# Optimization experiments

Hardware: AMD Instinct MI355X
Metric: run time of the kernel (lower is better)

The kernel has to match this reference:

```python
import jax, jax.numpy as jnp
import numpy as np

N, D, H = 2048, 1024, 16
HD = D // H  # 64
SCALE = float(np.sqrt(HD))  # sqrt(features // heads) = 8.0


def setup_inputs() -> dict:
    key = jax.random.key(0)
    ks = jax.random.split(key, 9)
    s = 0.02
    return {
        "x": jax.random.normal(ks[0], (N, D), dtype=jnp.float32),
        "Wq": jax.random.normal(ks[1], (D, D), dtype=jnp.float32) * s,
        "bq": jnp.zeros((D,), dtype=jnp.float32),
        "Wk": jax.random.normal(ks[2], (D, D), dtype=jnp.float32) * s,
        "bk": jnp.zeros((D,), dtype=jnp.float32),
        "Wv": jax.random.normal(ks[3], (D, D), dtype=jnp.float32) * s,
        "bv": jnp.zeros((D,), dtype=jnp.float32),
        "Wo": jax.random.normal(ks[4], (D, D), dtype=jnp.float32) * s,
        "bo": jnpp if False else jnp.zeros((D,), dtype=jnp.float32),
    }


def reference(x, Wq, bq, Wk, bk, Wv, bv, Wo, bo):
    # projections: [n, d]
    q = x @ Wq + bq
    k = x @ Wk + bk
    v = x @ Wv + bv
    # split heads: n (h d) -> h n d
    def split(t):
        return t.reshape(N, H, HD).transpose(1, 0, 2)
    q, k, v = split(q), split(k), split(v)
    # attention scores [h, n, n]
    scores = jnp.einsum('hnd,hmd->hnm', q, k) / SCALE
    # causal mask (tril), fill with dtype min as in original
    dmin = jnp.finfo(scores.dtype).min
    mask = jnp.tril(jnp.ones((N, N), dtype=bool))
    scores = jnp.where(mask, scores, dmin)
    attn = jax.nn.softmax(scores, axis=-1)
    # weighted sum, merge heads: h n d -> n (h d)
    out = jnp.einsum('hnm,hmd->hnd', attn, v)
    out = out.transpose(1, 0, 2).reshape(N, D)
    return out @ Wo + bo
```

## Files before the change

kernel.cpp:

```cpp
#include <hip/hip_runtime.h>
#include <hip/hip_bf16.h>
#include <math.h>

#define SA_N 2048
#define SA_D 1024
#define SA_H 16
#define SA_HD 64

typedef __attribute__((ext_vector_type(8))) short bf16x8;
typedef __attribute__((ext_vector_type(4))) float f32x4;
typedef __attribute__((address_space(3))) void lds_t;
typedef __attribute__((address_space(1))) void gmem_t;

#define SC2 0.18033688011112042f

__global__ __launch_bounds__(256) void prep_kernel(
    const float* __restrict__ x,
    const float* __restrict__ Wq, const float* __restrict__ Wk,
    const float* __restrict__ Wv, const float* __restrict__ Wo,
    __hip_bfloat16* __restrict__ xbf, __hip_bfloat16* __restrict__ WtAll)
{
    const int tid = threadIdx.x;
    const int z = blockIdx.z;
    if (z < 2) {
        const int r = z * 1024 + blockIdx.y * 32 + (tid >> 3);
        const int c = blockIdx.x * 32 + (tid & 7) * 4;
        const size_t idx = (size_t)r * SA_D + c;
        float4 v = *reinterpret_cast<const float4*>(&x[idx]);
        union { __hip_bfloat16 hh[4]; short4 s4; } u;
        u.hh[0] = __float2bfloat16(v.x);
        u.hh[1] = __float2bfloat16(v.y);
        u.hh[2] = __float2bfloat16(v.z);
        u.hh[3] = __float2bfloat16(v.w);
        *reinterpret_cast<short4*>(&xbf[idx]) = u.s4;
    } else {
        const int w = z - 2;
        const float* W = (w == 0) ? Wq : (w == 1) ? Wk : (w == 2) ? Wv : Wo;
        const float scale = (w == 0) ? SC2 : 1.0f;
        __hip_bfloat16* Wt = WtAll + (size_t)w * SA_D * SA_D;
        __shared__ float t[32][33];
        const int c0 = blockIdx.x * 32, r0 = blockIdx.y * 32;
        const int tx = tid & 31, ty = tid >> 5;
#pragma unroll
        for (int p = 0; p < 4; ++p)
            t[ty + p * 8][tx] = W[(size_t)(r0 + ty + p * 8) * SA_D + c0 + tx] * scale;
        __syncthreads();
#pragma unroll
        for (int p = 0; p < 4; ++p)
            Wt[(size_t)(c0 + ty + p * 8) * SA_D + r0 + tx] =
                __float2bfloat16(t[tx][ty + p * 8]);
    }
}

__global__ __launch_bounds__(256) void gemm_qkv_kernel(
    const __hip_bfloat16* __restrict__ xbf, const __hip_bfloat16* __restrict__ WtAll,
    const float* __restrict__ bq, const float* __restrict__ bk, const float* __restrict__ bv,
    __hip_bfloat16* __restrict__ Qb, __hip_bfloat16* __restrict__ Kb,
    __hip_bfloat16* __restrict__ VtT)
{
    __shared__ __align__(16) char As[64 * 128];
    __shared__ __align__(16) char Bs[3][32 * 128];

    const int tid = threadIdx.x;
    const int wave = tid >> 6, lane = tid & 63;
    const int m = lane & 15, quad = lane >> 4;
    const int wm = wave >> 1, wn = wave & 1;
    const int row0 = blockIdx.y * 64, col0 = blockIdx.x * 32;

    f32x4 acc[3][2];
#pragma unroll
    for (int w = 0; w < 3; ++w)
#pragma unroll
        for (int mi = 0; mi < 2; ++mi) acc[w][mi] = (f32x4){0.f, 0.f, 0.f, 0.f};

    const int sr = tid >> 3;
    const int sc = tid & 7;

    for (int k0 = 0; k0 < SA_D; k0 += 64) {
#pragma unroll
        for (int p = 0; p < 2; ++p) {
            const int r = p * 32 + sr;
            const int pc = (sc ^ (r & 7)) * 16;
            const char* ga = (const char*)(xbf + (size_t)(row0 + r) * SA_D + k0) + pc;
            __builtin_amdgcn_global_load_lds((gmem_t*)ga,
                (lds_t*)(As + p * 4096 + wave * 1024), 16, 0, 0);
        }
#pragma unroll
        for (int w = 0; w < 3; ++w) {
            const int pc = (sc ^ (sr & 7)) * 16;
            const char* gb = (const char*)(WtAll + (size_t)w * SA_D * SA_D
                                           + (size_t)(col0 + sr) * SA_D + k0) + pc;
            __builtin_amdgcn_global_load_lds((gmem_t*)gb,
                (lds_t*)(Bs[w] + wave * 1024), 16, 0, 0);
        }
        __syncthreads();

#pragma unroll
        for (int s = 0; s < 2; ++s) {
            bf16x8 af[2];
#pragma unroll
            for (int mi = 0; mi < 2; ++mi) {
                const int row = wm * 32 + mi * 16 + m;
                const int pc = (s * 4 + quad) ^ (row & 7);
                af[mi] = *reinterpret_cast<const bf16x8*>(As + row * 128 + pc * 16);
            }
            const int rb = wn * 16 + m;
            const int pcb = (s * 4 + quad) ^ (rb & 7);
#pragma unroll
            for (int w = 0; w < 3; ++w) {
                bf16x8 bf = *reinterpret_cast<const bf16x8*>(Bs[w] + rb * 128 + pcb * 16);
#pragma unroll
                for (int mi = 0; mi < 2; ++mi)
                    acc[w][mi] = __builtin_amdgcn_mfma_f32_16x16x32_bf16(
                        af[mi], bf, acc[w][mi], 0, 0, 0);
            }
        }
        __syncthreads();
    }

    const int col = col0 + wn * 16 + m;
    const float bvq = bq[col] * SC2, bvk = bk[col], bvv = bv[col];
#pragma unroll
    for (int mi = 0; mi < 2; ++mi) {
        const int rbase = row0 + wm * 32 + mi * 16 + quad * 4;
#pragma unroll
        for (int reg = 0; reg < 4; ++reg) {
            Qb[(size_t)(rbase + reg) * SA_D + col] = __float2bfloat16(acc[0][mi][reg] + bvq);
            Kb[(size_t)(rbase + reg) * SA_D + col] = __float2bfloat16(acc[1][mi][reg] + bvk);
        }
#pragma unroll
        for (int reg = 0; reg < 4; ++reg) {
            const int jp = (quad * 4 + reg) * 4 + (wm * 2 + mi);
            VtT[(size_t)col * SA_N + row0 + jp] = __float2bfloat16(acc[2][mi][reg] + bvv);
        }
    }
}

__global__ __launch_bounds__(256) void gemm_out_kernel(
    const __hip_bfloat16* __restrict__ A, const __hip_bfloat16* __restrict__ Bt,
    const float* __restrict__ bias, float* __restrict__ Cout)
{
    __shared__ __align__(16) char As[64 * 128];
    __shared__ __align__(16) char Bs[64 * 128];
    const int tid = threadIdx.x;
    const int wave = tid >> 6, lane = tid & 63;
    const int m = lane & 15, quad = lane >> 4;
    const int wm = wave >> 1, wn = wave & 1;
    const int row0 = blockIdx.y * 64, col0 = blockIdx.x * 64;

    f32x4 acc[2][2];
#pragma unroll
    for (int i = 0; i < 2; ++i)
#pragma unroll
        for (int j = 0; j < 2; ++j) acc[i][j] = (f32x4){0.f, 0.f, 0.f, 0.f};

    const int sr = tid >> 3;
    const int sc = tid & 7;

    for (int k0 = 0; k0 < SA_D; k0 += 64) {
#pragma unroll
        for (int p = 0; p < 2; ++p) {
            const int r = p * 32 + sr;
            const int pc = (sc ^ (r & 7)) * 16;
            const char* ga = (const char*)(A + (size_t)(row0 + r) * SA_D + k0) + pc;
            __builtin_amdgcn_global_load_lds((gmem_t*)ga,
                (lds_t*)(As + p * 4096 + wave * 1024), 16, 0, 0);
            const char* gb = (const char*)(Bt + (size_t)(col0 + r) * SA_D + k0) + pc;
            __builtin_amdgcn_global_load_lds((gmem_t*)gb,
                (lds_t*)(Bs + p * 4096 + wave * 1024), 16, 0, 0);
        }
        __syncthreads();

#pragma unroll
        for (int s = 0; s < 2; ++s) {
            bf16x8 af[2], bfr[2];
#pragma unroll
            for (int mi = 0; mi < 2; ++mi) {
                const int row = wm * 32 + mi * 16 + m;
                const int pc = (s * 4 + quad) ^ (row & 7);
                af[mi] = *reinterpret_cast<const bf16x8*>(As + row * 128 + pc * 16);
            }
#pragma unroll
            for (int ni = 0; ni < 2; ++ni) {
                const int col = wn * 32 + ni * 16 + m;
                const int pc = (s * 4 + quad) ^ (col & 7);
                bfr[ni] = *reinterpret_cast<const bf16x8*>(Bs + col * 128 + pc * 16);
            }
#pragma unroll
            for (int mi = 0; mi < 2; ++mi)
#pragma unroll
                for (int ni = 0; ni < 2; ++ni)
                    acc[mi][ni] = __builtin_amdgcn_mfma_f32_16x16x32_bf16(
                        af[mi], bfr[ni], acc[mi][ni], 0, 0, 0);
        }
        __syncthreads();
    }

#pragma unroll
    for (int ni = 0; ni < 2; ++ni) {
        const int col = col0 + wn * 32 + ni * 16 + m;
        const float bv = bias[col];
#pragma unroll
        for (int mi = 0; mi < 2; ++mi) {
            const int rbase = row0 + wm * 32 + mi * 16 + quad * 4;
#pragma unroll
            for (int reg = 0; reg < 4; ++reg)
                Cout[(size_t)(rbase + reg) * SA_D + col] = acc[mi][ni][reg] + bv;
        }
    }
}

__global__ __launch_bounds__(512, 4) void flash_mfma_kernel(
    const __hip_bfloat16* __restrict__ Qb,
    const __hip_bfloat16* __restrict__ Kb,
    const __hip_bfloat16* __restrict__ Vt,
    __hip_bfloat16* __restrict__ O)
{
    const int b = blockIdx.x;
    const int h = b & 15;
    const int qraw = b >> 4;
    const int qt = (qraw < 16) ? qraw : 47 - qraw;
    const int row0 = qt * 64;
    const int ntiles = (qt >> 1) + 1;

    const int tid = threadIdx.x;
    const int wave = tid >> 6, lane = tid & 63;
    const int g = wave >> 2, w4 = wave & 3;
    const int ln = lane & 15, quad = lane >> 4;

    __shared__ __align__(16) char Qs[64 * 128];
    __shared__ __align__(16) char Ks[128 * 128];
    __shared__ __align__(16) char Vs[64 * 256];
    __shared__ __align__(16) char Ps[2][64 * 144];
    __shared__ float lmerge[64];

    {
        const int r = wave * 8 + (lane >> 3);
        const int pc = ((lane & 7) ^ (r & 7)) * 16;
        const char* gq = (const char*)(Qb + (size_t)(row0 + r) * SA_D + h * SA_HD) + pc;
        __builtin_amdgcn_global_load_lds((gmem_t*)gq,
            (lds_t*)(Qs + wave * 1024), 16, 0, 0);
    }

    const int kr0 = wave * 8 + (lane >> 3);
    const int kpc = ((lane & 7) ^ (kr0 & 7)) * 16;
    const int vr0 = wave * 4 + (lane >> 4);
    const int vpc = ((lane & 15) ^ (vr0 & 15)) * 16;
    bf16x8 kreg[2], vreg[2];

    auto prefetch = [&](int kt) {
#pragma unroll
        for (int p = 0; p < 2; ++p) {
            kreg[p] = *reinterpret_cast<const bf16x8*>(
                (const char*)(Kb + (size_t)(kt * 128 + p * 64 + kr0) * SA_D + h * SA_HD) + kpc);
            vreg[p] = *reinterpret_cast<const bf16x8*>(
                (const char*)(Vt + (size_t)(h * SA_HD + p * 32 + vr0) * SA_N + kt * 128) + vpc);
        }
    };
    prefetch(0);

    f32x4 oacc[4], lacc;
#pragma unroll
    for (int dg = 0; dg < 4; ++dg) oacc[dg] = (f32x4){0.f, 0.f, 0.f, 0.f};
    lacc = (f32x4){0.f, 0.f, 0.f, 0.f};

    const short one_bf = (short)0x3F80;
    const bf16x8 ones = {one_bf, one_bf, one_bf, one_bf, one_bf, one_bf, one_bf, one_bf};

    for (int kt = 0; kt < ntiles; ++kt) {
        __syncthreads();
#pragma unroll
        for (int p = 0; p < 2; ++p) {
            *reinterpret_cast<bf16x8*>(Ks + p * 8192 + wave * 1024 + lane * 16) = kreg[p];
            *reinterpret_cast<bf16x8*>(Vs + p * 8192 + wave * 1024 + lane * 16) = vreg[p];
        }
        __syncthreads();
        if (kt + 1 < ntiles) prefetch(kt + 1);

        f32x4 sacc[4];
#pragma unroll
        for (int gg = 0; gg < 4; ++gg) sacc[gg] = (f32x4){0.f, 0.f, 0.f, 0.f};
        const int mrow = w4 * 16 + ln;
#pragma unroll
        for (int s = 0; s < 2; ++s) {
            const int pca = (s * 4 + quad) ^ (mrow & 7);
            bf16x8 af = *reinterpret_cast<const bf16x8*>(Qs + mrow * 128 + pca * 16);
#pragma unroll
            for (int gg = 0; gg < 4; ++gg) {
                const int krow = g * 64 + gg * 16 + ln;
                const int pcb = (s * 4 + quad) ^ (krow & 7);
                bf16x8 bf = *reinterpret_cast<const bf16x8*>(Ks + krow * 128 + pcb * 16);
                sacc[gg] = __builtin_amdgcn_mfma_f32_16x16x32_bf16(af, bf, sacc[gg], 0, 0, 0);
            }
        }

        const bool last = (kt == ntiles - 1);
        const int prow_b = w4 * 16 + quad * 4;
        const int qrow_b = row0 + prow_b;
        char* Pg = Ps[g];
#pragma unroll
        for (int reg = 0; reg < 4; ++reg) {
            union { __hip_bfloat16 hh[4]; short4 s4; } u;
#pragma unroll
            for (int gg = 0; gg < 4; ++gg) {
                const int key = kt * 128 + g * 64 + gg * 16 + ln;
                float p = exp2f(sacc[gg][reg]);
                if (last && key > (qrow_b + reg)) p = 0.f;
                u.hh[gg] = __float2bfloat16(p);
            }
            *reinterpret_cast<short4*>(Pg + (prow_b + reg) * 144 + ln * 8) = u.s4;
        }

#pragma unroll
        for (int s2 = 0; s2 < 2; ++s2) {
            bf16x8 pf = *reinterpret_cast<const bf16x8*>(
                Pg + (w4 * 16 + ln) * 144 + s2 * 64 + quad * 16);
            lacc = __builtin_amdgcn_mfma_f32_16x16x32_bf16(pf, ones, lacc, 0, 0, 0);
#pragma unroll
            for (int dg = 0; dg < 4; ++dg) {
                const int vrow = dg * 16 + ln;
                const int kc = g * 8 + s2 * 4 + quad;
                const int pcb = (kc ^ (vrow & 15)) * 16;
                bf16x8 vf = *reinterpret_cast<const bf16x8*>(Vs + vrow * 256 + pcb);
                oacc[dg] = __builtin_amdgcn_mfma_f32_16x16x32_bf16(pf, vf, oacc[dg], 0, 0, 0);
            }
        }
    }

    __syncthreads();
    float* Kf = reinterpret_cast<float*>(Ks);
    if (g == 1) {
#pragma unroll
        for (int reg = 0; reg < 4; ++reg) {
            const int row = w4 * 16 + quad * 4 + reg;
#pragma unroll
            for (int dg = 0; dg < 4; ++dg)
                Kf[row * 64 + dg * 16 + ln] = oacc[dg][reg];
            if (ln == 0) lmerge[row] = lacc[reg];
        }
    }
    __syncthreads();
    if (g == 0) {
#pragma unroll
        for (int reg = 0; reg < 4; ++reg) {
            const int row = w4 * 16 + quad * 4 + reg;
            const float inv = 1.0f / (lacc[reg] + lmerge[row]);
            const int qrow = row0 + row;
#pragma unroll
            for (int dg = 0; dg < 4; ++dg)
                O[(size_t)qrow * SA_D + h * SA_HD + dg * 16 + ln] =
                    __float2bfloat16((oacc[dg][reg] + Kf[row * 64 + dg * 16 + ln]) * inv);
        }
    }
}

extern "C" void kernel_launch(void* const* d_in, const int* in_sizes, int n_in,
                              void* d_out, int out_size, void* d_ws, size_t ws_size,
                              hipStream_t stream) {
    const float* x  = (const float*)d_in[0];
    const float* Wq = (const float*)d_in[1];
    const float* bq = (const float*)d_in[2];
    const float* Wk = (const float*)d_in[3];
    const float* bk = (const float*)d_in[4];
    const float* Wv = (const float*)d_in[5];
    const float* bv = (const float*)d_in[6];
    const float* Wo = (const float*)d_in[7];
    const float* bo = (const float*)d_in[8];
    float* out = (float*)d_out;

    const size_t ND = (size_t)SA_N * SA_D;
    const size_t DD = (size_t)SA_D * SA_D;
    __hip_bfloat16* xbf   = (__hip_bfloat16*)d_ws;
    __hip_bfloat16* WtAll = xbf + ND;
    __hip_bfloat16* Qb    = WtAll + 4 * DD;
    __hip_bfloat16* Kb    = Qb + ND;
    __hip_bfloat16* VtT   = Kb + ND;
    __hip_bfloat16* Abf   = VtT + ND;

    prep_kernel<<<dim3(32, 32, 6), 256, 0, stream>>>(x, Wq, Wk, Wv, Wo, xbf, WtAll);
    gemm_qkv_kernel<<<dim3(SA_D / 32, SA_N / 64), 256, 0, stream>>>(
        xbf, WtAll, bq, bk, bv, Qb, Kb, VtT);
    flash_mfma_kernel<<<dim3(512), 512, 0, stream>>>(Qb, Kb, VtT, Abf);
    gemm_out_kernel<<<dim3(SA_D / 64, SA_N / 64), 256, 0, stream>>>(
        Abf, WtAll + 3 * DD, bo, out);
}
```

Before: 142.7 us.

## Retile QKV GEMM to 128x64 tiles over concatenated Q/K/V columns

The QKV projection kernel now treats the three weight matrices as one concatenated 3072-column output. Each block computes a 128x64 tile of a single weight, instead of a 64x32 tile replicated across all three weights. Each wave now holds a 4x2 grid of MFMA accumulators, which raises reuse of each LDS fragment and cuts redundant loads of the A matrix. The epilogue branches on which weight the block covers to write Q, K, or the permuted transposed V. The grid shrinks to 768 blocks, which may lower occupancy and load balance across CUs.

```diff
diff --git a/kernel.cpp b/kernel.cpp
--- a/kernel.cpp
+++ b/kernel.cpp
@@ -58,27 +58,31 @@
     __hip_bfloat16* __restrict__ Qb, __hip_bfloat16* __restrict__ Kb,
     __hip_bfloat16* __restrict__ VtT)
 {
-    __shared__ __align__(16) char As[64 * 128];
-    __shared__ __align__(16) char Bs[3][32 * 128];
+    __shared__ __align__(16) char As[128 * 128];
+    __shared__ __align__(16) char Bs[64 * 128];
 
     const int tid = threadIdx.x;
     const int wave = tid >> 6, lane = tid & 63;
     const int m = lane & 15, quad = lane >> 4;
     const int wm = wave >> 1, wn = wave & 1;
-    const int row0 = blockIdx.y * 64, col0 = blockIdx.x * 32;
-
-    f32x4 acc[3][2];
-#pragma unroll
-    for (int w = 0; w < 3; ++w)
-#pragma unroll
-        for (int mi = 0; mi < 2; ++mi) acc[w][mi] = (f32x4){0.f, 0.f, 0.f, 0.f};
+    const int row0 = blockIdx.y * 128;
+    const int col0 = blockIdx.x * 64;
+    const int w = col0 >> 10;
+    const int cw0 = col0 & 1023;
+    const __hip_bfloat16* Bt = WtAll + (size_t)w * SA_D * SA_D;
+
+    f32x4 acc[4][2];
+#pragma unroll
+    for (int mi = 0; mi < 4; ++mi)
+#pragma unroll
+        for (int ni = 0; ni < 2; ++ni) acc[mi][ni] = (f32x4){0.f, 0.f, 0.f, 0.f};
 
     const int sr = tid >> 3;
     const int sc = tid & 7;
 
     for (int k0 = 0; k0 < SA_D; k0 += 64) {
 #pragma unroll
-        for (int p = 0; p < 2; ++p) {
+        for (int p = 0; p < 4; ++p) {
             const int r = p * 32 + sr;
             const int pc = (sc ^ (r & 7)) * 16;
             const char* ga = (const char*)(xbf + (size_t)(row0 + r) * SA_D + k0) + pc;
@@ -86,52 +90,72 @@
                 (lds_t*)(As + p * 4096 + wave * 1024), 16, 0, 0);
         }
 #pragma unroll
-        for (int w = 0; w < 3; ++w) {
-            const int pc = (sc ^ (sr & 7)) * 16;
-            const char* gb = (const char*)(WtAll + (size_t)w * SA_D * SA_D
-                                           + (size_t)(col0 + sr) * SA_D + k0) + pc;
+        for (int p = 0; p < 2; ++p) {
+            const int r = p * 32 + sr;
+            const int pc = (sc ^ (r & 7)) * 16;
+            const char* gb = (const char*)(Bt + (size_t)(cw0 + r) * SA_D + k0) + pc;
             __builtin_amdgcn_global_load_lds((gmem_t*)gb,
-                (lds_t*)(Bs[w] + wave * 1024), 16, 0, 0);
+                (lds_t*)(Bs + p * 4096 + wave * 1024), 16, 0, 0);
         }
         __syncthreads();
 
 #pragma unroll
         for (int s = 0; s < 2; ++s) {
-            bf16x8 af[2];
-#pragma unroll
-            for (int mi = 0; mi < 2; ++mi) {
-                const int row = wm * 32 + mi * 16 + m;
+            bf16x8 af[4], bfr[2];
+#pragma unroll
+            for (int mi = 0; mi < 4; ++mi) {
+                const int row = wm * 64 + mi * 16 + m;
                 const int pc = (s * 4 + quad) ^ (row & 7);
                 af[mi] = *reinterpret_cast<const bf16x8*>(As + row * 128 + pc * 16);
             }
-            const int rb = wn * 16 + m;
-            const int pcb = (s * 4 + quad) ^ (rb & 7);
-#pragma unroll
-            for (int w = 0; w < 3; ++w) {
-                bf16x8 bf = *reinterpret_cast<const bf16x8*>(Bs[w] + rb * 128 + pcb * 16);
-#pragma unroll
-                for (int mi = 0; mi < 2; ++mi)
-                    acc[w][mi] = __builtin_amdgcn_mfma_f32_16x16x32_bf16(
-                        af[mi], bf, acc[w][mi], 0, 0, 0);
-            }
-        }
-        __syncthreads();
-    }
-
-    const int col = col0 + wn * 16 + m;
-    const float bvq = bq[col] * SC2, bvk = bk[col], bvv = bv[col];
-#pragma unroll
-    for (int mi = 0; mi < 2; ++mi) {
-        const int rbase = row0 + wm * 32 + mi * 16 + quad * 4;
-#pragma unroll
-        for (int reg = 0; reg < 4; ++reg) {
-            Qb[(size_t)(rbase + reg) * SA_D + col] = __float2bfloat16(acc[0][mi][reg] + bvq);
-            Kb[(size_t)(rbase + reg) * SA_D + col] = __float2bfloat16(acc[1][mi][reg] + bvk);
-        }
-#pragma unroll
-        for (int reg = 0; reg < 4; ++reg) {
-            const int jp = (quad * 4 + reg) * 4 + (wm * 2 + mi);
-            VtT[(size_t)col * SA_N + row0 + jp] = __float2bfloat16(acc[2][mi][reg] + bvv);
+#pragma unroll
+            for (int ni = 0; ni < 2; ++ni) {
+                const int col = wn * 32 + ni * 16 + m;
+                const int pc = (s * 4 + quad) ^ (col & 7);
+                bfr[ni] = *reinterpret_cast<const bf16x8*>(Bs + col * 128 + pc * 16);
+            }
+#pragma unroll
+            for (int mi = 0; mi < 4; ++mi)
+#pragma unroll
+                for (int ni = 0; ni < 2; ++ni)
+                    acc[mi][ni] = __builtin_amdgcn_mfma_f32_16x16x32_bf16(
+                        af[mi], bfr[ni], acc[mi][ni], 0, 0, 0);
+        }
+        __syncthreads();
+    }
+
+    if (w < 2) {
+        __hip_bfloat16* Out = w ? Kb : Qb;
+        const float* bb = w ? bk : bq;
+        const float bscale = w ? 1.0f : SC2;
+#pragma unroll
+        for (int ni = 0; ni < 2; ++ni) {
+            const int cw = cw0 + wn * 32 + ni * 16 + m;
+            const float bvv = bb[cw] * bscale;
+#pragma unroll
+            for (int mi = 0; mi < 4; ++mi) {
+                const int rbase = row0 + wm * 64 + mi * 16 + quad * 4;
+#pragma unroll
+                for (int reg = 0; reg < 4; ++reg)
+                    Out[(size_t)(rbase + reg) * SA_D + cw] =
+                        __float2bfloat16(acc[mi][ni][reg] + bvv);
+            }
+        }
+    } else {
+#pragma unroll
+        for (int ni = 0; ni < 2; ++ni) {
+            const int cw = cw0 + wn * 32 + ni * 16 + m;
+            const float bvv = bv[cw];
+            const int kblk = row0 + wm * 64;
+#pragma unroll
+            for (int mi = 0; mi < 4; ++mi) {
+#pragma unroll
+                for (int reg = 0; reg < 4; ++reg) {
+                    const int jp = (quad * 4 + reg) * 4 + mi;
+                    VtT[(size_t)cw * SA_N + kblk + jp] =
+                        __float2bfloat16(acc[mi][ni][reg] + bvv);
+                }
+            }
         }
     }
 }
@@ -378,7 +402,7 @@
     __hip_bfloat16* Abf   = VtT + ND;
 
     prep_kernel<<<dim3(32, 32, 6), 256, 0, stream>>>(x, Wq, Wk, Wv, Wo, xbf, WtAll);
-    gemm_qkv_kernel<<<dim3(SA_D / 32, SA_N / 64), 256, 0, stream>>>(
+    gemm_qkv_kernel<<<dim3(3072 / 64, SA_N / 128), 256, 0, stream>>>(
         xbf, WtAll, bq, bk, bv, Qb, Kb, VtT);
     flash_mfma_kernel<<<dim3(512), 512, 0, stream>>>(Qb, Kb, VtT, Abf);
     gemm_out_kernel<<<dim3(SA_D / 64, SA_N / 64), 256, 0, stream>>>(
```

Result: faster. 139.1 us (-2.5%).
